# Optimization experiments

Measured on AMD Instinct MI355X. Metric: run time of the kernel, lower is better.

Reference implementation:

```python
import jax, jax.numpy as jnp
import numpy as np

B, C, H, W = 4, 32, 512, 1024  # input feature map
HO, WO = 512, 1024             # output grid


def setup_inputs() -> dict:
    key = jax.random.key(0)
    k1, k2 = jax.random.split(key)
    x = jax.random.normal(k1, (B, C, H, W), dtype=jnp.float32)
    # real-valued (x, y) output coordinates for every input pixel, in-bounds
    scale = jnp.asarray([WO - 1, HO - 1], dtype=jnp.float32)
    sample_map = jax.random.uniform(k2, (H, W, 2), dtype=jnp.float32) * scale
    return {"x": x, "sample_map": sample_map, "out_h": HO, "out_w": WO}


def reference(x, sample_map, out_h, out_w):
    """Bilinear splat: scatter each input pixel x[:,:,i,j] into the output
    at real-valued location sample_map[i,j] = (x_coord, y_coord)."""
    b, c, h, w = x.shape
    n = h * w
    coords = sample_map.reshape(n, 2)
    cx, cy = coords[:, 0], coords[:, 1]
    x0 = jnp.floor(cx)
    y0 = jnp.floor(cy)
    wx = cx - x0  # fractional offsets
    wy = cy - y0
    x0i = x0.astype(jnp.int32)
    y0i = y0.astype(jnp.int32)

    vals = x.reshape(b, c, n)
    out = jnp.zeros((b, c, out_h * out_w), dtype=x.dtype)
    # four bilinear corners: (xi, yi, weight)
    corners = (
        (x0i,     y0i,     (1.0 - wx) * (1.0 - wy)),
        (x0i + 1, y0i,     wx * (1.0 - wy)),
        (x0i,     y0i + 1, (1.0 - wx) * wy),
        (x0i + 1, y0i + 1, wx * wy),
    )
    for xi, yi, wgt in corners:
        valid = (xi >= 0) & (xi < out_w) & (yi >= 0) & (yi < out_h)
        idx = jnp.where(valid, yi * out_w + xi, 0)              # [n]
        wgt = jnp.where(valid, wgt, 0.0).astype(x.dtype)        # [n]
        out = out.at[:, :, idx].add(vals * wgt)
    return out.reshape(b, c, out_h, out_w)
```

## Files before the change

kernel.cpp:

```cpp
#include <hip/hip_runtime.h>

constexpr int Bc   = 4;
constexpr int Cc   = 32;
constexpr int Hc   = 512;
constexpr int Wc   = 1024;
constexpr int HOc  = 512;
constexpr int WOc  = 1024;
constexpr int NPIX  = Hc * Wc;
constexpr int PLANE = HOc * WOc;
constexpr int BCn   = Bc * Cc;

constexpr int TH = 32, TW = 32;
constexpr int TILES_X = WOc / TW;
constexpr int TILES_Y = HOc / TH;
constexpr int NT = TILES_X * TILES_Y;
constexpr int G  = 8;
constexpr int CG = BCn / G;
constexpr int LDSW   = TW + 1;
constexpr int TCELLS = (TH + 1) * (TW + 1);

__device__ __forceinline__ int tile_of(float cx, float cy, int& x0, int& y0) {
    x0 = (int)floorf(cx);
    y0 = (int)floorf(cy);
    int tx = min(max(x0 >> 5, 0), TILES_X - 1);
    int ty = min(max(y0 >> 5, 0), TILES_Y - 1);
    return ty * TILES_X + tx;
}

__global__ __launch_bounds__(256) void hist_kernel(
    const float2* __restrict__ smap, int* __restrict__ count)
{
    __shared__ int h[NT];
    for (int i = threadIdx.x; i < NT; i += 256) h[i] = 0;
    __syncthreads();
    const int stride = gridDim.x * 256;
    for (int p = blockIdx.x * 256 + threadIdx.x; p < NPIX; p += stride) {
        float2 c = smap[p];
        int x0, y0;
        int t = tile_of(c.x, c.y, x0, y0);
        atomicAdd(&h[t], 1);
    }
    __syncthreads();
    for (int i = threadIdx.x; i < NT; i += 256)
        if (h[i]) atomicAdd(&count[i], h[i]);
}

__global__ __launch_bounds__(512) void scan_kernel(
    const int* __restrict__ count, int* __restrict__ off)
{
    __shared__ int s[NT];
    int tid = threadIdx.x;
    s[tid] = count[tid];
    __syncthreads();
    for (int d = 1; d < NT; d <<= 1) {
        int v = (tid >= d) ? s[tid - d] : 0;
        __syncthreads();
        s[tid] += v;
        __syncthreads();
    }
    if (tid == 0) off[0] = 0;
    off[tid + 1] = s[tid];
}

__global__ __launch_bounds__(256) void scatter_pos_kernel(
    const float2* __restrict__ smap, const int* __restrict__ off,
    int* __restrict__ cursor, int* __restrict__ pos,
    float2* __restrict__ smap_g)
{
    __shared__ int h[NT];
    __shared__ int base[NT];
    const int tid = threadIdx.x;
    for (int i = tid; i < NT; i += 256) h[i] = 0;
    __syncthreads();
    const int p = blockIdx.x * 256 + tid;
    const float2 c = smap[p];
    int x0, y0;
    const int t = tile_of(c.x, c.y, x0, y0);
    atomicAdd(&h[t], 1);
    __syncthreads();
    for (int i = tid; i < NT; i += 256) {
        int cnt = h[i];
        base[i] = cnt ? atomicAdd(&cursor[i], cnt) : 0;
        h[i] = 0;
    }
    __syncthreads();
    const int r = atomicAdd(&h[t], 1);
    const int posi = off[t] + base[t] + r;
    pos[p] = posi;
    smap_g[posi] = c;
}

__global__ __launch_bounds__(256) void gather_kernel(
    const float* __restrict__ x, const int* __restrict__ pos,
    float* __restrict__ xg, int cg0, int ncg)
{
    const int p = (blockIdx.x * 256 + threadIdx.x) * 4;
    const int4 d = *reinterpret_cast<const int4*>(pos + p);
    for (int g = 0; g < ncg; ++g) {
        const float* xp = x + (long)(cg0 + g) * G * NPIX + p;
        float4 r[8];
#pragma unroll
        for (int k = 0; k < 8; ++k)
            r[k] = *reinterpret_cast<const float4*>(xp + (long)k * NPIX);
        float* o0 = xg + ((long)g * NPIX + d.x) * 8;
        float* o1 = xg + ((long)g * NPIX + d.y) * 8;
        float* o2 = xg + ((long)g * NPIX + d.z) * 8;
        float* o3 = xg + ((long)g * NPIX + d.w) * 8;
        *reinterpret_cast<float4*>(o0)     = make_float4(r[0].x, r[1].x, r[2].x, r[3].x);
        *reinterpret_cast<float4*>(o0 + 4) = make_float4(r[4].x, r[5].x, r[6].x, r[7].x);
        *reinterpret_cast<float4*>(o1)     = make_float4(r[0].y, r[1].y, r[2].y, r[3].y);
        *reinterpret_cast<float4*>(o1 + 4) = make_float4(r[4].y, r[5].y, r[6].y, r[7].y);
        *reinterpret_cast<float4*>(o2)     = make_float4(r[0].z, r[1].z, r[2].z, r[3].z);
        *reinterpret_cast<float4*>(o2 + 4) = make_float4(r[4].z, r[5].z, r[6].z, r[7].z);
        *reinterpret_cast<float4*>(o3)     = make_float4(r[0].w, r[1].w, r[2].w, r[3].w);
        *reinterpret_cast<float4*>(o3 + 4) = make_float4(r[4].w, r[5].w, r[6].w, r[7].w);
    }
}

__global__ __launch_bounds__(256) void accum_kernel(
    const float*  __restrict__ xg,
    const float2* __restrict__ smap_g,
    const int*    __restrict__ off,
    float*        __restrict__ out,
    int cg0)
{
    __shared__ float acc[G][TCELLS];
    const int t     = blockIdx.x;
    const int gslab = blockIdx.y;
    const int bc0   = (cg0 + gslab) * G;
    const int tx0 = (t % TILES_X) * TW;
    const int ty0 = (t / TILES_X) * TH;
    const int tid = threadIdx.x;

    for (int i = tid; i < G * TCELLS; i += 256)
        (&acc[0][0])[i] = 0.0f;
    __syncthreads();

    const int lo = off[t], n = off[t + 1] - lo;
    const float* xs = xg + (long)gslab * NPIX * 8;
    for (int i = tid; i < n; i += 256) {
        const float2 c = smap_g[lo + i];
        const float x0f = floorf(c.x);
        const float y0f = floorf(c.y);
        const float wx = c.x - x0f;
        const float wy = c.y - y0f;
        const int lx = (int)x0f - tx0;
        const int ly = (int)y0f - ty0;
        if ((unsigned)lx >= (unsigned)TW || (unsigned)ly >= (unsigned)TH) continue;
        const float w00 = (1.0f - wx) * (1.0f - wy);
        const float w10 = wx * (1.0f - wy);
        const float w01 = (1.0f - wx) * wy;
        const float w11 = wx * wy;
        const int a = ly * LDSW + lx;
        const float4 va = *reinterpret_cast<const float4*>(xs + (long)(lo + i) * 8);
        const float4 vb = *reinterpret_cast<const float4*>(xs + (long)(lo + i) * 8 + 4);
        const float v[8] = {va.x, va.y, va.z, va.w, vb.x, vb.y, vb.z, vb.w};
#pragma unroll
        for (int k = 0; k < G; ++k) {
            atomicAdd(&acc[k][a],            v[k] * w00);
            atomicAdd(&acc[k][a + 1],        v[k] * w10);
            atomicAdd(&acc[k][a + LDSW],     v[k] * w01);
            atomicAdd(&acc[k][a + LDSW + 1], v[k] * w11);
        }
    }
    __syncthreads();

    for (int idx = tid; idx < TCELLS; idx += 256) {
        const int r = idx / LDSW;
        const int cc = idx - r * LDSW;
        const int gy = ty0 + r, gx = tx0 + cc;
        if (gy >= HOc || gx >= WOc) continue;
        const bool edge = (r == 0) | (cc == 0) | (r == TH) | (cc == TW);
        const long o = (long)gy * WOc + gx;
#pragma unroll
        for (int k = 0; k < G; ++k) {
            const float v = acc[k][idx];
            float* op = out + (long)(bc0 + k) * PLANE + o;
            if (edge) { if (v != 0.0f) unsafeAtomicAdd(op, v); }
            else      { *op = v; }
        }
    }
}

__global__ __launch_bounds__(256) void splat_kernel(
    const float* __restrict__ x, const float2* __restrict__ smap,
    float* __restrict__ out)
{
    const int p = blockIdx.x * blockDim.x + threadIdx.x;
    if (p >= NPIX) return;
    const float2 c = smap[p];
    const float x0f = floorf(c.x), y0f = floorf(c.y);
    const float wx = c.x - x0f, wy = c.y - y0f;
    const int x0 = (int)x0f, y0 = (int)y0f;
    const float w00 = (1.0f-wx)*(1.0f-wy), w10 = wx*(1.0f-wy);
    const float w01 = (1.0f-wx)*wy, w11 = wx*wy;
    const bool vx0 = (x0>=0)&(x0<WOc), vx1 = (x0+1>=0)&(x0+1<WOc);
    const bool vy0 = (y0>=0)&(y0<HOc), vy1 = (y0+1>=0)&(y0+1<HOc);
    const long base = (long)y0*WOc + x0;
    const int bc0 = blockIdx.y * 4;
#pragma unroll
    for (int k = 0; k < 4; ++k) {
        const int bc = bc0 + k;
        const float v = x[(long)bc*NPIX + p];
        float* o = out + (long)bc*PLANE;
        if (vx0 & vy0) unsafeAtomicAdd(o + base,          v*w00);
        if (vx1 & vy0) unsafeAtomicAdd(o + base + 1,      v*w10);
        if (vx0 & vy1) unsafeAtomicAdd(o + base + WOc,    v*w01);
        if (vx1 & vy1) unsafeAtomicAdd(o + base + WOc+1,  v*w11);
    }
}

extern "C" void kernel_launch(void* const* d_in, const int* in_sizes, int n_in,
                              void* d_out, int out_size, void* d_ws, size_t ws_size,
                              hipStream_t stream) {
    const float*  x    = (const float*)d_in[0];
    const float2* smap = (const float2*)d_in[1];
    float*        out  = (float*)d_out;

    hipMemsetAsync(d_out, 0, (size_t)out_size * sizeof(float), stream);

    const size_t int_bytes  = sizeof(int) * ((size_t)NPIX + 3 * NT + 1);
    size_t ofs = (int_bytes + 255) & ~(size_t)255;
    const size_t smapg_ofs = ofs;
    ofs += sizeof(float2) * (size_t)NPIX;
    ofs = (ofs + 255) & ~(size_t)255;
    const size_t xg_ofs = ofs;
    const size_t slab_bytes = (size_t)NPIX * G * sizeof(float);

    long slabs = 0;
    if (ws_size > xg_ofs) slabs = (long)((ws_size - xg_ofs) / slab_bytes);
    if (slabs > CG) slabs = CG;

    if (slabs < 1) {
        dim3 grid(NPIX / 256, BCn / 4);
        splat_kernel<<<grid, 256, 0, stream>>>(x, smap, out);
        return;
    }

    char* wsb      = (char*)d_ws;
    int*  pos      = (int*)wsb;
    int*  count    = pos + NPIX;
    int*  cursor   = count + NT;
    int*  off      = cursor + NT;
    float2* smap_g = (float2*)(wsb + smapg_ofs);
    float*  xg     = (float*)(wsb + xg_ofs);

    hipMemsetAsync(count, 0, sizeof(int) * 2 * NT, stream);

    hist_kernel       <<<256, 256, 0, stream>>>(smap, count);
    scan_kernel       <<<1, 512, 0, stream>>>(count, off);
    scatter_pos_kernel<<<NPIX / 256, 256, 0, stream>>>(smap, off, cursor, pos, smap_g);

    for (int cg0 = 0; cg0 < CG; cg0 += (int)slabs) {
        int ncg = CG - cg0;
        if (ncg > slabs) ncg = (int)slabs;
        gather_kernel<<<NPIX / 1024, 256, 0, stream>>>(x, pos, xg, cg0, ncg);
        dim3 grid2(NT, ncg);
        accum_kernel <<<grid2, 256, 0, stream>>>(xg, smap_g, off, out, cg0);
    }
}
```

Measured before the change: 2.187 ms.

## Replace LDS atomic splat with per-cell gather lists built once per tile

Adds a cellbuild kernel that, for each output tile, buckets the four bilinear contributions of every source pixel by destination cell (a CSR of pixel index plus weight). The accum kernel then stages the tile's values, entries and weights in shared memory and lets each thread sum its cell's contributions in registers, removing shared-memory float atomics. Pixels beyond a per-tile cap or outside the tile fall back to global atomics. This adds an extra pass and workspace for entries, uses a larger shared-memory footprint and 512-thread blocks, and changes the order of the floating-point summation.

```diff
diff --git a/kernel.cpp b/kernel.cpp
--- a/kernel.cpp
+++ b/kernel.cpp
@@ -18,6 +18,9 @@
 constexpr int CG = BCn / G;
 constexpr int LDSW   = TW + 1;
 constexpr int TCELLS = (TH + 1) * (TW + 1);
+constexpr int NBIN   = TCELLS + 1;
+constexpr int NMAX   = 1280;
+constexpr int EMAX   = 4 * NMAX;
 
 __device__ __forceinline__ int tile_of(float cx, float cy, int& x0, int& y0) {
     x0 = (int)floorf(cx);
@@ -88,6 +91,92 @@
     const int posi = off[t] + base[t] + r;
     pos[p] = posi;
     smap_g[posi] = c;
+}
+
+__global__ __launch_bounds__(256) void cellbuild_kernel(
+    const float2* __restrict__ smap_g, const int* __restrict__ off,
+    ushort* __restrict__ ent, float* __restrict__ entw,
+    int* __restrict__ gcello)
+{
+    __shared__ unsigned cnt[NBIN];
+    __shared__ unsigned coff[NBIN + 1];
+    __shared__ unsigned psum[256];
+    const int t   = blockIdx.x;
+    const int tx0 = (t % TILES_X) * TW;
+    const int ty0 = (t / TILES_X) * TH;
+    const int lo  = off[t];
+    const int n   = off[t + 1] - lo;
+    const int nn  = min(n, NMAX);
+    const int tid = threadIdx.x;
+
+    for (int i = tid; i < NBIN; i += 256) cnt[i] = 0;
+    __syncthreads();
+
+    for (int i = tid; i < nn; i += 256) {
+        float2 c = smap_g[lo + i];
+        int x0 = (int)floorf(c.x), y0 = (int)floorf(c.y);
+        int lx = x0 - tx0, ly = y0 - ty0;
+        if ((unsigned)lx < (unsigned)TW && (unsigned)ly < (unsigned)TH) {
+            int a = ly * LDSW + lx;
+            atomicAdd(&cnt[a], 1u);
+            atomicAdd(&cnt[a + 1], 1u);
+            atomicAdd(&cnt[a + LDSW], 1u);
+            atomicAdd(&cnt[a + LDSW + 1], 1u);
+        } else {
+            atomicAdd(&cnt[TCELLS], 1u);
+        }
+    }
+    __syncthreads();
+
+    constexpr int BPT = (NBIN + 255) / 256;
+    unsigned loc[BPT];
+    unsigned s = 0;
+    for (int j = 0; j < BPT; ++j) {
+        int b = tid * BPT + j;
+        unsigned v = (b < NBIN) ? cnt[b] : 0u;
+        loc[j] = s; s += v;
+    }
+    psum[tid] = s;
+    __syncthreads();
+    for (int d = 1; d < 256; d <<= 1) {
+        unsigned v = (tid >= d) ? psum[tid - d] : 0u;
+        __syncthreads();
+        psum[tid] += v;
+        __syncthreads();
+    }
+    unsigned base = (tid > 0) ? psum[tid - 1] : 0u;
+    for (int j = 0; j < BPT; ++j) {
+        int b = tid * BPT + j;
+        if (b < NBIN) coff[b] = base + loc[j];
+    }
+    if (tid == 255) coff[NBIN] = psum[255];
+    __syncthreads();
+
+    for (int i = tid; i < NBIN; i += 256) cnt[i] = coff[i];
+    for (int i = tid; i < NBIN + 1; i += 256)
+        gcello[t * (NBIN + 1) + i] = (int)coff[i];
+    __syncthreads();
+
+    const int ebase = 4 * lo;
+    for (int i = tid; i < nn; i += 256) {
+        float2 c = smap_g[lo + i];
+        float fx = floorf(c.x), fy = floorf(c.y);
+        float wx = c.x - fx, wy = c.y - fy;
+        int lx = (int)fx - tx0, ly = (int)fy - ty0;
+        if ((unsigned)lx < (unsigned)TW && (unsigned)ly < (unsigned)TH) {
+            int a = ly * LDSW + lx;
+            float w00 = (1.f - wx) * (1.f - wy), w10 = wx * (1.f - wy);
+            float w01 = (1.f - wx) * wy,         w11 = wx * wy;
+            unsigned e;
+            e = atomicAdd(&cnt[a], 1u);            ent[ebase + e] = (ushort)i; entw[ebase + e] = w00;
+            e = atomicAdd(&cnt[a + 1], 1u);        ent[ebase + e] = (ushort)i; entw[ebase + e] = w10;
+            e = atomicAdd(&cnt[a + LDSW], 1u);     ent[ebase + e] = (ushort)i; entw[ebase + e] = w01;
+            e = atomicAdd(&cnt[a + LDSW + 1], 1u); ent[ebase + e] = (ushort)i; entw[ebase + e] = w11;
+        } else {
+            unsigned e = atomicAdd(&cnt[TCELLS], 1u);
+            ent[ebase + e] = (ushort)i; entw[ebase + e] = 0.f;
+        }
+    }
 }
 
 __global__ __launch_bounds__(256) void gather_kernel(
@@ -117,67 +206,109 @@
     }
 }
 
-__global__ __launch_bounds__(256) void accum_kernel(
+__global__ __launch_bounds__(512) void accum_kernel(
     const float*  __restrict__ xg,
     const float2* __restrict__ smap_g,
     const int*    __restrict__ off,
-    float*        __restrict__ out,
-    int cg0)
-{
-    __shared__ float acc[G][TCELLS];
+    const ushort* __restrict__ ent,
+    const float*  __restrict__ entw,
+    const int*    __restrict__ gcello,
+    float*        __restrict__ out, int cg0)
+{
+    __shared__ float4   vals4[2 * NMAX];
+    __shared__ float    wl[EMAX];
+    __shared__ unsigned entl[EMAX / 2];
+    __shared__ unsigned offl[NBIN + 1];
     const int t     = blockIdx.x;
     const int gslab = blockIdx.y;
     const int bc0   = (cg0 + gslab) * G;
     const int tx0 = (t % TILES_X) * TW;
     const int ty0 = (t / TILES_X) * TH;
     const int tid = threadIdx.x;
-
-    for (int i = tid; i < G * TCELLS; i += 256)
-        (&acc[0][0])[i] = 0.0f;
-    __syncthreads();
-
-    const int lo = off[t], n = off[t + 1] - lo;
+    const int lo = off[t], n = off[t + 1] - lo, nn = min(n, NMAX);
     const float* xs = xg + (long)gslab * NPIX * 8;
-    for (int i = tid; i < n; i += 256) {
-        const float2 c = smap_g[lo + i];
-        const float x0f = floorf(c.x);
-        const float y0f = floorf(c.y);
-        const float wx = c.x - x0f;
-        const float wy = c.y - y0f;
-        const int lx = (int)x0f - tx0;
-        const int ly = (int)y0f - ty0;
-        if ((unsigned)lx >= (unsigned)TW || (unsigned)ly >= (unsigned)TH) continue;
-        const float w00 = (1.0f - wx) * (1.0f - wy);
-        const float w10 = wx * (1.0f - wy);
-        const float w01 = (1.0f - wx) * wy;
-        const float w11 = wx * wy;
-        const int a = ly * LDSW + lx;
-        const float4 va = *reinterpret_cast<const float4*>(xs + (long)(lo + i) * 8);
-        const float4 vb = *reinterpret_cast<const float4*>(xs + (long)(lo + i) * 8 + 4);
-        const float v[8] = {va.x, va.y, va.z, va.w, vb.x, vb.y, vb.z, vb.w};
-#pragma unroll
-        for (int k = 0; k < G; ++k) {
-            atomicAdd(&acc[k][a],            v[k] * w00);
-            atomicAdd(&acc[k][a + 1],        v[k] * w10);
-            atomicAdd(&acc[k][a + LDSW],     v[k] * w01);
-            atomicAdd(&acc[k][a + LDSW + 1], v[k] * w11);
-        }
-    }
-    __syncthreads();
-
-    for (int idx = tid; idx < TCELLS; idx += 256) {
-        const int r = idx / LDSW;
-        const int cc = idx - r * LDSW;
+
+    const float4* vsrc = (const float4*)(xs + (long)lo * 8);
+    for (int j = tid; j < nn * 2; j += 512) vals4[j] = vsrc[j];
+    const unsigned* esrc = (const unsigned*)(ent + 4 * lo);
+    for (int j = tid; j < nn * 2; j += 512) entl[j] = esrc[j];
+    const float* wsrc = entw + 4 * lo;
+    for (int j = tid; j < nn * 4; j += 512) wl[j] = wsrc[j];
+    for (int j = tid; j < NBIN + 1; j += 512) offl[j] = (unsigned)gcello[t * (NBIN + 1) + j];
+    __syncthreads();
+
+    const ushort* entl16 = (const ushort*)entl;
+
+    for (int c = tid; c < TCELLS; c += 512) {
+        const unsigned e0 = offl[c], e1 = offl[c + 1];
+        float a0 = 0, a1 = 0, a2 = 0, a3 = 0, a4 = 0, a5 = 0, a6 = 0, a7 = 0;
+        for (unsigned e = e0; e < e1; ++e) {
+            const int idx = entl16[e];
+            const float w = wl[e];
+            const float4 va = vals4[idx * 2];
+            const float4 vb = vals4[idx * 2 + 1];
+            a0 += va.x * w; a1 += va.y * w; a2 += va.z * w; a3 += va.w * w;
+            a4 += vb.x * w; a5 += vb.y * w; a6 += vb.z * w; a7 += vb.w * w;
+        }
+        const int r = c / LDSW, cc = c - r * LDSW;
         const int gy = ty0 + r, gx = tx0 + cc;
         if (gy >= HOc || gx >= WOc) continue;
         const bool edge = (r == 0) | (cc == 0) | (r == TH) | (cc == TW);
         const long o = (long)gy * WOc + gx;
-#pragma unroll
-        for (int k = 0; k < G; ++k) {
-            const float v = acc[k][idx];
+        const float av[8] = {a0, a1, a2, a3, a4, a5, a6, a7};
+#pragma unroll
+        for (int k = 0; k < 8; ++k) {
             float* op = out + (long)(bc0 + k) * PLANE + o;
-            if (edge) { if (v != 0.0f) unsafeAtomicAdd(op, v); }
-            else      { *op = v; }
+            if (edge) { if (av[k] != 0.0f) unsafeAtomicAdd(op, av[k]); }
+            else      { *op = av[k]; }
+        }
+    }
+    __syncthreads();
+
+    {
+        const unsigned e0 = offl[TCELLS], e1 = offl[NBIN];
+        for (unsigned e = e0 + tid; e < e1; e += 512) {
+            const int idx = entl16[e];
+            const float2 c2 = smap_g[lo + idx];
+            const float fx = floorf(c2.x), fy = floorf(c2.y);
+            const float wx = c2.x - fx, wy = c2.y - fy;
+            const int x0 = (int)fx, y0 = (int)fy;
+            const float4 va = vals4[idx * 2], vb = vals4[idx * 2 + 1];
+            const float v[8] = {va.x, va.y, va.z, va.w, vb.x, vb.y, vb.z, vb.w};
+            const float cw[4] = {(1.f - wx) * (1.f - wy), wx * (1.f - wy),
+                                 (1.f - wx) * wy,         wx * wy};
+            const int cxs[4] = {x0, x0 + 1, x0, x0 + 1};
+            const int cys[4] = {y0, y0, y0 + 1, y0 + 1};
+#pragma unroll
+            for (int q = 0; q < 4; ++q) {
+                if (cxs[q] < 0 || cxs[q] >= WOc || cys[q] < 0 || cys[q] >= HOc) continue;
+                const long o = (long)cys[q] * WOc + cxs[q];
+#pragma unroll
+                for (int k = 0; k < 8; ++k)
+                    unsafeAtomicAdd(out + (long)(bc0 + k) * PLANE + o, v[k] * cw[q]);
+            }
+        }
+    }
+
+    for (int i = NMAX + tid; i < n; i += 512) {
+        const float2 c2 = smap_g[lo + i];
+        const float fx = floorf(c2.x), fy = floorf(c2.y);
+        const float wx = c2.x - fx, wy = c2.y - fy;
+        const int x0 = (int)fx, y0 = (int)fy;
+        const float4 va = *((const float4*)(xs + (long)(lo + i) * 8));
+        const float4 vb = *((const float4*)(xs + (long)(lo + i) * 8) + 1);
+        const float v[8] = {va.x, va.y, va.z, va.w, vb.x, vb.y, vb.z, vb.w};
+        const float cw[4] = {(1.f - wx) * (1.f - wy), wx * (1.f - wy),
+                             (1.f - wx) * wy,         wx * wy};
+        const int cxs[4] = {x0, x0 + 1, x0, x0 + 1};
+        const int cys[4] = {y0, y0, y0 + 1, y0 + 1};
+#pragma unroll
+        for (int q = 0; q < 4; ++q) {
+            if (cxs[q] < 0 || cxs[q] >= WOc || cys[q] < 0 || cys[q] >= HOc) continue;
+            const long o = (long)cys[q] * WOc + cxs[q];
+#pragma unroll
+            for (int k = 0; k < 8; ++k)
+                unsafeAtomicAdd(out + (long)(bc0 + k) * PLANE + o, v[k] * cw[q]);
         }
     }
 }
@@ -219,10 +350,16 @@
 
     hipMemsetAsync(d_out, 0, (size_t)out_size * sizeof(float), stream);
 
-    const size_t int_bytes  = sizeof(int) * ((size_t)NPIX + 3 * NT + 1);
-    size_t ofs = (int_bytes + 255) & ~(size_t)255;
+    const size_t ints = (size_t)NPIX + 3 * NT + 1 + (size_t)NT * (NBIN + 1);
+    size_t ofs = (ints * sizeof(int) + 255) & ~(size_t)255;
     const size_t smapg_ofs = ofs;
     ofs += sizeof(float2) * (size_t)NPIX;
+    ofs = (ofs + 255) & ~(size_t)255;
+    const size_t ent_ofs = ofs;
+    ofs += sizeof(ushort) * 4 * (size_t)NPIX;
+    ofs = (ofs + 255) & ~(size_t)255;
+    const size_t entw_ofs = ofs;
+    ofs += sizeof(float) * 4 * (size_t)NPIX;
     ofs = (ofs + 255) & ~(size_t)255;
     const size_t xg_ofs = ofs;
     const size_t slab_bytes = (size_t)NPIX * G * sizeof(float);
@@ -242,7 +379,10 @@
     int*  count    = pos + NPIX;
     int*  cursor   = count + NT;
     int*  off      = cursor + NT;
+    int*  gcello   = off + NT + 1;
     float2* smap_g = (float2*)(wsb + smapg_ofs);
+    ushort* ent    = (ushort*)(wsb + ent_ofs);
+    float*  entw   = (float*)(wsb + entw_ofs);
     float*  xg     = (float*)(wsb + xg_ofs);
 
     hipMemsetAsync(count, 0, sizeof(int) * 2 * NT, stream);
@@ -250,12 +390,13 @@
     hist_kernel       <<<256, 256, 0, stream>>>(smap, count);
     scan_kernel       <<<1, 512, 0, stream>>>(count, off);
     scatter_pos_kernel<<<NPIX / 256, 256, 0, stream>>>(smap, off, cursor, pos, smap_g);
+    cellbuild_kernel  <<<NT, 256, 0, stream>>>(smap_g, off, ent, entw, gcello);
 
     for (int cg0 = 0; cg0 < CG; cg0 += (int)slabs) {
         int ncg = CG - cg0;
         if (ncg > slabs) ncg = (int)slabs;
         gather_kernel<<<NPIX / 1024, 256, 0, stream>>>(x, pos, xg, cg0, ncg);
         dim3 grid2(NT, ncg);
-        accum_kernel <<<grid2, 256, 0, stream>>>(xg, smap_g, off, out, cg0);
-    }
-}
+        accum_kernel <<<grid2, 512, 0, stream>>>(xg, smap_g, off, ent, entw, gcello, out, cg0);
+    }
+}
```

After: 1.981 ms. -9.4%, faster.
